# Kernel optimization log

Hardware: AMD Instinct MI355X
Metric: run time of the kernel (lower is better)

The kernel has to match this reference:

```python
import jax, jax.numpy as jnp
import numpy as np

B, L, D, M = 8, 4096, 512, 64


def setup_inputs() -> dict:
    key = jax.random.key(0)
    k1, k2, k3 = jax.random.split(key, 3)
    scale = 1.0 / (D * D)
    return {
        "q": jax.random.normal(k1, (B, L, D), dtype=jnp.float32),
        "w_real": scale * jax.random.normal(k2, (D, D, M), dtype=jnp.float32),
        "w_imag": scale * jax.random.normal(k3, (D, D, M), dtype=jnp.float32),
    }


def reference(q, w_real, w_imag):
    # q: [B, L, D]; weights: [D, D, modes]
    b, l, d = q.shape
    n_freq = l // 2 + 1
    q_ft = jnp.fft.rfft(q, axis=1)                      # [B, n_freq, D] complex64
    m = min(w_real.shape[-1], n_freq)
    W = w_real[..., :m] + 1j * w_imag[..., :m]          # [D, E, m] complex
    # Batched over modes: replaces the per-mode python loop with one einsum.
    out_m = jnp.einsum('bmd,dem->bme', q_ft[:, :m, :], W)  # [B, m, D]
    out_ft = jnp.zeros((b, n_freq, d), dtype=q_ft.dtype).at[:, :m, :].set(out_m)
    return jnp.fft.irfft(out_ft, n=l, axis=1)           # [B, L, D] float32
```

## Files before the change

### kernel.cpp

```cpp
#include <hip/hip_runtime.h>

#define B_ 8
#define L_ 4096
#define D_ 512
#define M_ 64

typedef __attribute__((ext_vector_type(8))) short bh8;
typedef __attribute__((ext_vector_type(4))) float f4;
typedef __attribute__((ext_vector_type(4))) unsigned u32x4;

__device__ inline unsigned short f2bf(float f) {
  unsigned u = __float_as_uint(f);
  return (unsigned short)((u + 0x7fffu + ((u >> 16) & 1u)) >> 16);
}
__device__ inline unsigned packbf(float lo, float hi) {
  return (unsigned)f2bf(lo) | ((unsigned)f2bf(hi) << 16);
}

__global__ void k_ftab(unsigned short* __restrict__ F) {
  int t = blockIdx.x * 256 + threadIdx.x;
  int r = t >> 12, l = t & 4095;
  int k = r & 63, part = r >> 6;
  int ph = (k * l) & (L_ - 1);
  double ang = 6.283185307179586476925286766559 * (double)ph / (double)L_;
  float v = part ? (float)(-sin(ang)) : (float)(cos(ang));
  F[t] = f2bf(v);
}

__global__ void k_gtab(unsigned short* __restrict__ G) {
  int t = blockIdx.x * 256 + threadIdx.x;
  int l = t >> 7, j = t & 127;
  int k = j & 63, part = j >> 6;
  int ph = (k * l) & (L_ - 1);
  double ang = 6.283185307179586476925286766559 * (double)ph / (double)L_;
  double ck = (k == 0 ? 1.0 : 2.0) / (double)L_;
  float v = part ? (float)(-ck * sin(ang)) : (float)(ck * cos(ang));
  G[t] = f2bf(v);
}

__global__ __launch_bounds__(512, 4) void k_dft_mfma(
    const float* __restrict__ q, const unsigned short* __restrict__ F,
    float* __restrict__ pQ) {
  int tid = threadIdx.x;
  int dt = blockIdx.x, b = blockIdx.y, kc = blockIdx.z;
  int d0 = dt * 64;
  int lbase = kc * 512;

  int w = tid >> 6, lane = tid & 63;
  int mh = w & 3, nc = w >> 2;
  int lr = lane & 15, kg = lane >> 4;

  f4 acc[2][2];
#pragma unroll
  for (int i = 0; i < 2; ++i)
#pragma unroll
    for (int j = 0; j < 2; ++j) { f4 z = {0.f, 0.f, 0.f, 0.f}; acc[i][j] = z; }

  const unsigned short* A0 = F + (size_t)(mh * 32 + lr) * 4096 + lbase + kg * 8;
  const unsigned short* A1 = A0 + (size_t)16 * 4096;
  const float* q0 = q + ((size_t)b * L_ + lbase + kg * 8) * D_ + d0 + nc * 32 + lr;

#pragma unroll 2
  for (int s = 0; s < 16; ++s) {
    const float* qs = q0 + (size_t)s * 32 * D_;
    float v0[8], v1[8];
#pragma unroll
    for (int j = 0; j < 8; ++j) {
      v0[j] = qs[(size_t)j * D_];
      v1[j] = qs[(size_t)j * D_ + 16];
    }
    union { u32x4 u; bh8 h; } bf0, bf1;
    bf0.u.x = packbf(v0[0], v0[1]); bf0.u.y = packbf(v0[2], v0[3]);
    bf0.u.z = packbf(v0[4], v0[5]); bf0.u.w = packbf(v0[6], v0[7]);
    bf1.u.x = packbf(v1[0], v1[1]); bf1.u.y = packbf(v1[2], v1[3]);
    bf1.u.z = packbf(v1[4], v1[5]); bf1.u.w = packbf(v1[6], v1[7]);
    bh8 af0 = *(const bh8*)(A0 + s * 32);
    bh8 af1 = *(const bh8*)(A1 + s * 32);
    acc[0][0] = __builtin_amdgcn_mfma_f32_16x16x32_bf16(af0, bf0.h, acc[0][0], 0, 0, 0);
    acc[0][1] = __builtin_amdgcn_mfma_f32_16x16x32_bf16(af0, bf1.h, acc[0][1], 0, 0, 0);
    acc[1][0] = __builtin_amdgcn_mfma_f32_16x16x32_bf16(af1, bf0.h, acc[1][0], 0, 0, 0);
    acc[1][1] = __builtin_amdgcn_mfma_f32_16x16x32_bf16(af1, bf1.h, acc[1][1], 0, 0, 0);
  }

#pragma unroll
  for (int mi = 0; mi < 2; ++mi) {
    int r = mh * 32 + mi * 16 + kg * 4;
#pragma unroll
    for (int ni = 0; ni < 2; ++ni) {
      int d = d0 + nc * 32 + ni * 16 + lr;
#pragma unroll
      for (int j = 0; j < 4; ++j)
        pQ[(((size_t)kc * 128 + (r + j)) * 8 + b) * 512 + d] = acc[mi][ni][j];
    }
  }
}

__global__ __launch_bounds__(256) void k_red2(const float* __restrict__ pQ,
                                              unsigned* __restrict__ Qbf) {
  int g = blockIdx.x * 256 + threadIdx.x;
  int dq = g & 127;
  int b = (g >> 7) & 7;
  int k = g >> 10;
  f4 sr = {0.f, 0.f, 0.f, 0.f}, si = {0.f, 0.f, 0.f, 0.f};
#pragma unroll
  for (int kc = 0; kc < 8; ++kc) {
    size_t base = (((size_t)kc * 128 + k) * 8 + b) * 512 + dq * 4;
    sr += *(const f4*)(pQ + base);
    si += *(const f4*)(pQ + base + (size_t)64 * 8 * 512);
  }
  u32x4 o;
  o.x = packbf(sr[0], si[0]); o.y = packbf(sr[1], si[1]);
  o.z = packbf(sr[2], si[2]); o.w = packbf(sr[3], si[3]);
  *(u32x4*)(Qbf + ((size_t)k * 8 + b) * 512 + dq * 4) = o;
}

__global__ __launch_bounds__(512, 4) void k_mix_mfma(
    const float* __restrict__ wr_, const float* __restrict__ wi_,
    const unsigned* __restrict__ Qbf, float* __restrict__ pOut) {
  __shared__ unsigned Wt[16384];
  int tid = threadIdx.x;
  int et = blockIdx.x, dc = blockIdx.y;
  int e0 = et * 16;
  int w = tid >> 6, lane = tid & 63;
  int er = lane & 15, kg = lane >> 4;
  int part = er >> 3, b = er & 7;

  f4 acc[8];
#pragma unroll
  for (int t = 0; t < 8; ++t) { f4 z = {0.f, 0.f, 0.f, 0.f}; acc[t] = z; }

  for (int r = 0; r < 4; ++r) {
    if (r) __syncthreads();
    int dbase = dc * 64 + r * 16;
#pragma unroll
    for (int i = 0; i < 8; ++i) {
      int f = tid + i * 512;
      int d_loc = f >> 8;
      int e = (f >> 4) & 15;
      int k4 = f & 15;
      size_t gidx = ((size_t)(dbase + d_loc) * 512 + (e0 + e)) * 16 + k4;
      float4 a  = ((const float4*)wr_)[gidx];
      float4 bb = ((const float4*)wi_)[gidx];
      int dp = d_loc ^ ((k4 & 3) << 2);
      int base = k4 * 1024 + e * 16 + dp;
      Wt[base]       = packbf(a.x, bb.x);
      Wt[base + 256] = packbf(a.y, bb.y);
      Wt[base + 512] = packbf(a.z, bb.z);
      Wt[base + 768] = packbf(a.w, bb.w);
    }
    __syncthreads();
    int d0 = dbase + kg * 4;
#pragma unroll
    for (int t = 0; t < 8; ++t) {
      int k = w * 8 + t;
      int sw = ((k >> 2) & 3) << 2;
      union { u32x4 u; bh8 h; } av, bv;
      av.u = *(const u32x4*)&Wt[k * 256 + er * 16 + ((kg * 4) ^ sw)];
      u32x4 qv = *(const u32x4*)(Qbf + ((size_t)k * 8 + b) * 512 + d0);
      if (part == 0) {
        bv.u.x = qv.x ^ 0x80000000u; bv.u.y = qv.y ^ 0x80000000u;
        bv.u.z = qv.z ^ 0x80000000u; bv.u.w = qv.w ^ 0x80000000u;
      } else {
        bv.u.x = (qv.x >> 16) | (qv.x << 16); bv.u.y = (qv.y >> 16) | (qv.y << 16);
        bv.u.z = (qv.z >> 16) | (qv.z << 16); bv.u.w = (qv.w >> 16) | (qv.w << 16);
      }
      acc[t] = __builtin_amdgcn_mfma_f32_16x16x32_bf16(av.h, bv.h, acc[t], 0, 0, 0);
    }
  }

#pragma unroll
  for (int t = 0; t < 8; ++t) {
    int k = w * 8 + t;
    size_t off = (size_t)dc * 524288 +
                 (((size_t)k * 2 + part) * 8 + b) * 512 + e0 + kg * 4;
    *(f4*)(pOut + off) = acc[t];
  }
}

__global__ __launch_bounds__(256) void k_psum2(const float* __restrict__ pOut,
                                               unsigned* __restrict__ Pw) {
  __shared__ float sP[128 * 33];
  int tid = threadIdx.x;
  int e0 = blockIdx.x * 32, b = blockIdx.y;
  {
    int e = tid & 31, kg4 = tid >> 5;
#pragma unroll
    for (int ii = 0; ii < 16; ++ii) {
      int col = kg4 * 16 + ii;
      int rkp = ((col & 63) << 1) | (col >> 6);
      float s = 0.f;
#pragma unroll
      for (int c = 0; c < 8; ++c)
        s += pOut[(size_t)c * 524288 + (size_t)rkp * 4096 + b * 512 + e0 + e];
      sP[col * 33 + e] = s;
    }
  }
  __syncthreads();
  {
    int e = tid >> 3, c = tid & 7;
    size_t wbase = (((size_t)b * 512 + e0 + e) * 128 + c * 16) >> 1;
#pragma unroll
    for (int ii = 0; ii < 8; ++ii) {
      int col = c * 16 + ii * 2;
      Pw[wbase + ii] = packbf(sP[col * 33 + e], sP[(col + 1) * 33 + e]);
    }
  }
}

#define LST 72
__global__ __launch_bounds__(256, 2) void k_inv_mfma(
    const short* __restrict__ G, const short* __restrict__ P,
    float* __restrict__ y) {
  __shared__ short lds[2 * 128 * LST];
  short* As = lds;
  short* Bs = lds + 128 * LST;

  int tid = threadIdx.x;
  int lt = blockIdx.x, et = blockIdx.y, b = blockIdx.z;
  int l0 = lt * 128, e0 = et * 128;

  int wv = tid >> 6, lane = tid & 63;
  int wrow = wv >> 1, wcol = wv & 1;
  int lr = lane & 15, kg = lane >> 4;

  const short* Gb = G + (size_t)l0 * 128;
  const short* Pb = P + (size_t)b * D_ * 128 + (size_t)e0 * 128;

  f4 acc[4][4];
#pragma unroll
  for (int mi = 0; mi < 4; ++mi)
#pragma unroll
    for (int ni = 0; ni < 4; ++ni) {
      f4 z = {0.f, 0.f, 0.f, 0.f};
      acc[mi][ni] = z;
    }

#pragma unroll
  for (int kh = 0; kh < 2; ++kh) {
    if (kh) __syncthreads();
#pragma unroll
    for (int i = 0; i < 4; ++i) {
      int idx = i * 256 + tid;
      int row = idx >> 3, c = idx & 7;
      *(uint4*)(As + row * LST + c * 8) =
          *(const uint4*)(Gb + (size_t)row * 128 + kh * 64 + c * 8);
      *(uint4*)(Bs + row * LST + c * 8) =
          *(const uint4*)(Pb + (size_t)row * 128 + kh * 64 + c * 8);
    }
    __syncthreads();

#pragma unroll
    for (int ks = 0; ks < 2; ++ks) {
      bh8 a[4], bf[4];
#pragma unroll
      for (int i = 0; i < 4; ++i) {
        a[i]  = *(const bh8*)(As + (wrow * 64 + i * 16 + lr) * LST + ks * 32 + kg * 8);
        bf[i] = *(const bh8*)(Bs + (wcol * 64 + i * 16 + lr) * LST + ks * 32 + kg * 8);
      }
#pragma unroll
      for (int mi = 0; mi < 4; ++mi)
#pragma unroll
        for (int ni = 0; ni < 4; ++ni)
          acc[mi][ni] = __builtin_amdgcn_mfma_f32_16x16x32_bf16(
              a[mi], bf[ni], acc[mi][ni], 0, 0, 0);
    }
  }

#pragma unroll
  for (int mi = 0; mi < 4; ++mi) {
    int lg = l0 + wrow * 64 + mi * 16 + kg * 4;
#pragma unroll
    for (int ni = 0; ni < 4; ++ni) {
      int e = e0 + wcol * 64 + ni * 16 + lr;
#pragma unroll
      for (int j = 0; j < 4; ++j)
        y[((size_t)b * L_ + (lg + j)) * D_ + e] = acc[mi][ni][j];
    }
  }
}

extern "C" void kernel_launch(void* const* d_in, const int* in_sizes, int n_in,
                              void* d_out, int out_size, void* d_ws, size_t ws_size,
                              hipStream_t stream) {
  const float* q  = (const float*)d_in[0];
  const float* wr = (const float*)d_in[1];
  const float* wi = (const float*)d_in[2];
  float* out = (float*)d_out;
  char* ws = (char*)d_ws;

  unsigned short* Fbf = (unsigned short*)ws;
  unsigned short* Gbf = (unsigned short*)(ws + (1u << 20));
  unsigned* Qbf       = (unsigned*)(ws + (2u << 20));
  unsigned* Pw        = (unsigned*)(ws + (3u << 20));

  float* pQ   = out;
  float* pOut = out;

  hipLaunchKernelGGL(k_ftab, dim3((128 * L_) / 256), dim3(256), 0, stream, Fbf);
  hipLaunchKernelGGL(k_gtab, dim3((L_ * 128) / 256), dim3(256), 0, stream, Gbf);
  hipLaunchKernelGGL(k_dft_mfma, dim3(8, 8, 8), dim3(512), 0, stream,
                     q, Fbf, pQ);
  hipLaunchKernelGGL(k_red2, dim3(65536 / 256), dim3(256), 0, stream, pQ, Qbf);
  hipLaunchKernelGGL(k_mix_mfma, dim3(D_ / 16, 8), dim3(512), 0, stream,
                     wr, wi, Qbf, pOut);
  hipLaunchKernelGGL(k_psum2, dim3(16, 8), dim3(256), 0, stream, pOut, Pw);
  hipLaunchKernelGGL(k_inv_mfma, dim3(L_ / 128, D_ / 128, B_), dim3(256), 0,
                     stream, (const short*)Gbf, (const short*)Pw, out);
}
```

Before: 107.7 us.

## Double-buffer weight loads in mix kernel and split D reduction across more blocks

The mix kernel now covers 32 input channels per block instead of 64, which doubles the grid to 16 D-chunks so more blocks stream the 64 MB of weights in parallel. Inside each block, the global loads for the second 16-channel slab are issued into registers before the MFMA work on the first slab, so load latency overlaps compute. The partial-sum kernel now reduces 16 partial outputs instead of 8, which means more partial traffic through the output buffer. Register pressure also rises from holding 16 float4 values per thread.

```diff
diff --git a/kernel.cpp b/kernel.cpp
--- a/kernel.cpp
+++ b/kernel.cpp
@@ -125,48 +125,65 @@
   int er = lane & 15, kg = lane >> 4;
   int part = er >> 3, b = er & 7;
 
+  int e = (tid >> 4) & 15, k4 = tid & 15, dl0 = tid >> 8;
+  const float4* wr4p = (const float4*)wr_;
+  const float4* wi4p = (const float4*)wi_;
+  int dbase = dc * 32;
+
   f4 acc[8];
 #pragma unroll
   for (int t = 0; t < 8; ++t) { f4 z = {0.f, 0.f, 0.f, 0.f}; acc[t] = z; }
 
-  for (int r = 0; r < 4; ++r) {
-    if (r) __syncthreads();
-    int dbase = dc * 64 + r * 16;
-#pragma unroll
-    for (int i = 0; i < 8; ++i) {
-      int f = tid + i * 512;
-      int d_loc = f >> 8;
-      int e = (f >> 4) & 15;
-      int k4 = f & 15;
-      size_t gidx = ((size_t)(dbase + d_loc) * 512 + (e0 + e)) * 16 + k4;
-      float4 a  = ((const float4*)wr_)[gidx];
-      float4 bb = ((const float4*)wi_)[gidx];
-      int dp = d_loc ^ ((k4 & 3) << 2);
-      int base = k4 * 1024 + e * 16 + dp;
-      Wt[base]       = packbf(a.x, bb.x);
-      Wt[base + 256] = packbf(a.y, bb.y);
-      Wt[base + 512] = packbf(a.z, bb.z);
-      Wt[base + 768] = packbf(a.w, bb.w);
-    }
-    __syncthreads();
-    int d0 = dbase + kg * 4;
-#pragma unroll
-    for (int t = 0; t < 8; ++t) {
-      int k = w * 8 + t;
-      int sw = ((k >> 2) & 3) << 2;
-      union { u32x4 u; bh8 h; } av, bv;
-      av.u = *(const u32x4*)&Wt[k * 256 + er * 16 + ((kg * 4) ^ sw)];
-      u32x4 qv = *(const u32x4*)(Qbf + ((size_t)k * 8 + b) * 512 + d0);
-      if (part == 0) {
-        bv.u.x = qv.x ^ 0x80000000u; bv.u.y = qv.y ^ 0x80000000u;
-        bv.u.z = qv.z ^ 0x80000000u; bv.u.w = qv.w ^ 0x80000000u;
-      } else {
-        bv.u.x = (qv.x >> 16) | (qv.x << 16); bv.u.y = (qv.y >> 16) | (qv.y << 16);
-        bv.u.z = (qv.z >> 16) | (qv.z << 16); bv.u.w = (qv.w >> 16) | (qv.w << 16);
-      }
-      acc[t] = __builtin_amdgcn_mfma_f32_16x16x32_bf16(av.h, bv.h, acc[t], 0, 0, 0);
-    }
-  }
+  float4 wrv[8], wiv[8];
+
+#define GOFF(dd) ((((size_t)(dd)*512) + e0 + e) * 16 + k4)
+#define LOADW(dstart)                                   \
+  _Pragma("unroll") for (int i = 0; i < 8; ++i) {       \
+    int dd = (dstart) + dl0 + 2 * i;                    \
+    wrv[i] = wr4p[GOFF(dd)];                            \
+    wiv[i] = wi4p[GOFF(dd)];                            \
+  }
+#define PACKW()                                         \
+  _Pragma("unroll") for (int i = 0; i < 8; ++i) {       \
+    int d_loc = dl0 + 2 * i;                            \
+    int dp = d_loc ^ ((k4 & 3) << 2);                   \
+    int base = k4 * 1024 + e * 16 + dp;                 \
+    Wt[base]       = packbf(wrv[i].x, wiv[i].x);        \
+    Wt[base + 256] = packbf(wrv[i].y, wiv[i].y);        \
+    Wt[base + 512] = packbf(wrv[i].z, wiv[i].z);        \
+    Wt[base + 768] = packbf(wrv[i].w, wiv[i].w);        \
+  }
+#define COMPUTEW(dq)                                                        \
+  _Pragma("unroll") for (int t = 0; t < 8; ++t) {                           \
+    int k = w * 8 + t;                                                      \
+    int sw = ((k >> 2) & 3) << 2;                                           \
+    union { u32x4 u; bh8 h; } av, bv;                                       \
+    av.u = *(const u32x4*)&Wt[k * 256 + er * 16 + ((kg * 4) ^ sw)];         \
+    u32x4 qv = *(const u32x4*)(Qbf + ((size_t)k * 8 + b) * 512 + (dq) + kg * 4); \
+    if (part == 0) {                                                        \
+      bv.u.x = qv.x ^ 0x80000000u; bv.u.y = qv.y ^ 0x80000000u;             \
+      bv.u.z = qv.z ^ 0x80000000u; bv.u.w = qv.w ^ 0x80000000u;             \
+    } else {                                                                \
+      bv.u.x = (qv.x >> 16) | (qv.x << 16); bv.u.y = (qv.y >> 16) | (qv.y << 16); \
+      bv.u.z = (qv.z >> 16) | (qv.z << 16); bv.u.w = (qv.w >> 16) | (qv.w << 16); \
+    }                                                                       \
+    acc[t] = __builtin_amdgcn_mfma_f32_16x16x32_bf16(av.h, bv.h, acc[t], 0, 0, 0); \
+  }
+
+  LOADW(dbase);
+  PACKW();
+  __syncthreads();
+  LOADW(dbase + 16);
+  COMPUTEW(dbase);
+  __syncthreads();
+  PACKW();
+  __syncthreads();
+  COMPUTEW(dbase + 16);
+
+#undef GOFF
+#undef LOADW
+#undef PACKW
+#undef COMPUTEW
 
 #pragma unroll
   for (int t = 0; t < 8; ++t) {
@@ -190,7 +207,7 @@
       int rkp = ((col & 63) << 1) | (col >> 6);
       float s = 0.f;
 #pragma unroll
-      for (int c = 0; c < 8; ++c)
+      for (int c = 0; c < 16; ++c)
         s += pOut[(size_t)c * 524288 + (size_t)rkp * 4096 + b * 512 + e0 + e];
       sP[col * 33 + e] = s;
     }
@@ -301,7 +318,7 @@
   hipLaunchKernelGGL(k_dft_mfma, dim3(8, 8, 8), dim3(512), 0, stream,
                      q, Fbf, pQ);
   hipLaunchKernelGGL(k_red2, dim3(65536 / 256), dim3(256), 0, stream, pQ, Qbf);
-  hipLaunchKernelGGL(k_mix_mfma, dim3(D_ / 16, 8), dim3(512), 0, stream,
+  hipLaunchKernelGGL(k_mix_mfma, dim3(D_ / 16, 16), dim3(512), 0, stream,
                      wr, wi, Qbf, pOut);
   hipLaunchKernelGGL(k_psum2, dim3(16, 8), dim3(256), 0, stream, pOut, Pw);
   hipLaunchKernelGGL(k_inv_mfma, dim3(L_ / 128, D_ / 128, B_), dim3(256), 0,
```

Measured after the change: 127.3 us. 1.18x slower.

## Software-pipeline mode-mixing kernel with double-buffered LDS and split mode dimension

Applied to the files above, without the earlier changes.

Rewrites the weight-mixing MFMA kernel so each block handles half of the 64 modes, which doubles the grid and halves the per-block accumulators. Weight loads use inline-asm global loads that are double-buffered in LDS with manual vmcnt/lgkmcnt waits and barriers, so loading the next d-slice overlaps with the MFMA work on the current one. The load pattern also changes so each lane reads contiguous mode runs. The gain is more parallelism and hidden weight-streaming latency. The cost is fragile hand-counted waitcnts and inline asm that the compiler cannot schedule around.

```diff
diff --git a/kernel.cpp b/kernel.cpp
--- a/kernel.cpp
+++ b/kernel.cpp
@@ -117,62 +117,144 @@
 __global__ __launch_bounds__(512, 4) void k_mix_mfma(
     const float* __restrict__ wr_, const float* __restrict__ wi_,
     const unsigned* __restrict__ Qbf, float* __restrict__ pOut) {
-  __shared__ unsigned Wt[16384];
+  __shared__ unsigned Wt[2][8192];
+
   int tid = threadIdx.x;
-  int et = blockIdx.x, dc = blockIdx.y;
-  int e0 = et * 16;
+  int et = blockIdx.x, kh = blockIdx.y, dc = blockIdx.z;
+  int e0 = et * 16, D0 = dc * 64;
   int w = tid >> 6, lane = tid & 63;
   int er = lane & 15, kg = lane >> 4;
   int part = er >> 3, b = er & 7;
 
-  f4 acc[8];
-#pragma unroll
-  for (int t = 0; t < 8; ++t) { f4 z = {0.f, 0.f, 0.f, 0.f}; acc[t] = z; }
-
-  for (int r = 0; r < 4; ++r) {
-    if (r) __syncthreads();
-    int dbase = dc * 64 + r * 16;
-#pragma unroll
-    for (int i = 0; i < 8; ++i) {
-      int f = tid + i * 512;
-      int d_loc = f >> 8;
-      int e = (f >> 4) & 15;
-      int k4 = f & 15;
-      size_t gidx = ((size_t)(dbase + d_loc) * 512 + (e0 + e)) * 16 + k4;
-      float4 a  = ((const float4*)wr_)[gidx];
-      float4 bb = ((const float4*)wi_)[gidx];
-      int dp = d_loc ^ ((k4 & 3) << 2);
-      int base = k4 * 1024 + e * 16 + dp;
-      Wt[base]       = packbf(a.x, bb.x);
-      Wt[base + 256] = packbf(a.y, bb.y);
-      Wt[base + 512] = packbf(a.z, bb.z);
-      Wt[base + 768] = packbf(a.w, bb.w);
-    }
-    __syncthreads();
-    int d0 = dbase + kg * 4;
-#pragma unroll
-    for (int t = 0; t < 8; ++t) {
-      int k = w * 8 + t;
-      int sw = ((k >> 2) & 3) << 2;
-      union { u32x4 u; bh8 h; } av, bv;
-      av.u = *(const u32x4*)&Wt[k * 256 + er * 16 + ((kg * 4) ^ sw)];
-      u32x4 qv = *(const u32x4*)(Qbf + ((size_t)k * 8 + b) * 512 + d0);
-      if (part == 0) {
-        bv.u.x = qv.x ^ 0x80000000u; bv.u.y = qv.y ^ 0x80000000u;
-        bv.u.z = qv.z ^ 0x80000000u; bv.u.w = qv.w ^ 0x80000000u;
-      } else {
-        bv.u.x = (qv.x >> 16) | (qv.x << 16); bv.u.y = (qv.y >> 16) | (qv.y << 16);
-        bv.u.z = (qv.z >> 16) | (qv.z << 16); bv.u.w = (qv.w >> 16) | (qv.w << 16);
-      }
-      acc[t] = __builtin_amdgcn_mfma_f32_16x16x32_bf16(av.h, bv.h, acc[t], 0, 0, 0);
-    }
-  }
-
-#pragma unroll
-  for (int t = 0; t < 8; ++t) {
-    int k = w * 8 + t;
+  int e8 = lane >> 3, k4g = lane & 7;
+  int koff = kh * 32 + k4g * 4;
+  int swl = (k4g & 3) << 2;
+  int dloc0 = w * 2;
+
+  const unsigned* qlane =
+      Qbf + ((size_t)(kh * 32 + w * 4) * 8 + b) * 512 + D0 + kg * 4;
+
+  f4 acc[4];
+#pragma unroll
+  for (int t = 0; t < 4; ++t) { f4 z = {0.f, 0.f, 0.f, 0.f}; acc[t] = z; }
+
+  f4 LR0, LR1, LR2, LR3, LI0, LI1, LI2, LI3;
+  u32x4 QA0, QA1, QA2, QA3, QB0, QB1, QB2, QB3;
+
+#define GLD(dst, p) \
+  asm volatile("global_load_dwordx4 %0, %1, off" : "=v"(dst) : "v"(p))
+#define SB() __builtin_amdgcn_sched_barrier(0)
+#define VMW(n) do { asm volatile("s_waitcnt vmcnt(" #n ")" ::: "memory"); SB(); } while (0)
+#define LKM0() do { asm volatile("s_waitcnt lgkmcnt(0)" ::: "memory"); SB(); } while (0)
+#define BAR() do { __builtin_amdgcn_s_barrier(); SB(); } while (0)
+
+#define LOADL(r) do {                                                        \
+    size_t d_ = (size_t)(D0 + 16 * (r) + dloc0);                             \
+    const float* p00 = wr_ + (d_ * 512 + e0 + e8) * 64 + koff;               \
+    const float* p01 = wr_ + (d_ * 512 + e0 + 8 + e8) * 64 + koff;           \
+    const float* p10 = wr_ + ((d_ + 1) * 512 + e0 + e8) * 64 + koff;         \
+    const float* p11 = wr_ + ((d_ + 1) * 512 + e0 + 8 + e8) * 64 + koff;     \
+    const float* q00 = wi_ + (d_ * 512 + e0 + e8) * 64 + koff;               \
+    const float* q01 = wi_ + (d_ * 512 + e0 + 8 + e8) * 64 + koff;           \
+    const float* q10 = wi_ + ((d_ + 1) * 512 + e0 + e8) * 64 + koff;         \
+    const float* q11 = wi_ + ((d_ + 1) * 512 + e0 + 8 + e8) * 64 + koff;     \
+    GLD(LR0, p00); GLD(LR1, p01); GLD(LR2, p10); GLD(LR3, p11);              \
+    GLD(LI0, q00); GLD(LI1, q01); GLD(LI2, q10); GLD(LI3, q11);              \
+  } while (0)
+
+#define LOADQ(q0_, q1_, q2_, q3_, r) do {                                    \
+    GLD(q0_, (const float*)(qlane + (r) * 16));                              \
+    GLD(q1_, (const float*)(qlane + 4096 + (r) * 16));                       \
+    GLD(q2_, (const float*)(qlane + 8192 + (r) * 16));                       \
+    GLD(q3_, (const float*)(qlane + 12288 + (r) * 16));                      \
+  } while (0)
+
+#define PACK1(wb, vr, vi, dl, el) do {                                       \
+    int dp_ = (dl) ^ swl;                                                    \
+    unsigned* o_ = &Wt[wb][(k4g * 4) * 256 + (el) * 16 + dp_];               \
+    o_[0]   = packbf(vr[0], vi[0]);                                          \
+    o_[256] = packbf(vr[1], vi[1]);                                          \
+    o_[512] = packbf(vr[2], vi[2]);                                          \
+    o_[768] = packbf(vr[3], vi[3]);                                          \
+  } while (0)
+
+#define PACKL(wb) do {                                                      \
+    PACK1(wb, LR0, LI0, dloc0, e8);                                         \
+    PACK1(wb, LR1, LI1, dloc0, 8 + e8);                                     \
+    PACK1(wb, LR2, LI2, dloc0 + 1, e8);                                     \
+    PACK1(wb, LR3, LI3, dloc0 + 1, 8 + e8);                                 \
+  } while (0)
+
+#define COMPW(wb, q0_, q1_, q2_, q3_) do {                                  \
+    u32x4 qarr0 = q0_, qarr1 = q1_, qarr2 = q2_, qarr3 = q3_;               \
+    _Pragma("unroll") for (int t = 0; t < 4; ++t) {                         \
+      int kl_ = w * 4 + t;                                                  \
+      int sw_ = ((kl_ >> 2) & 3) << 2;                                      \
+      union { u32x4 u; bh8 h; } av, bv;                                     \
+      av.u = *(const u32x4*)&Wt[wb][kl_ * 256 + er * 16 + ((kg * 4) ^ sw_)]; \
+      u32x4 q = (t == 0) ? qarr0 : (t == 1) ? qarr1 : (t == 2) ? qarr2 : qarr3; \
+      if (part == 0) {                                                      \
+        bv.u.x = q.x ^ 0x80000000u; bv.u.y = q.y ^ 0x80000000u;             \
+        bv.u.z = q.z ^ 0x80000000u; bv.u.w = q.w ^ 0x80000000u;             \
+      } else {                                                              \
+        bv.u.x = (q.x >> 16) | (q.x << 16); bv.u.y = (q.y >> 16) | (q.y << 16); \
+        bv.u.z = (q.z >> 16) | (q.z << 16); bv.u.w = (q.w >> 16) | (q.w << 16); \
+      }                                                                     \
+      acc[t] = __builtin_amdgcn_mfma_f32_16x16x32_bf16(av.h, bv.h, acc[t], 0, 0, 0); \
+    }                                                                       \
+  } while (0)
+
+  LOADL(0);
+  VMW(0);
+  PACKL(0);
+  LOADL(1);
+  LOADQ(QA0, QA1, QA2, QA3, 0);
+
+  VMW(4);
+  PACKL(1);
+  LKM0(); BAR();
+  LOADL(2);
+  LOADQ(QB0, QB1, QB2, QB3, 1);
+  VMW(12);
+  COMPW(0, QA0, QA1, QA2, QA3);
+  LKM0(); BAR();
+
+  VMW(4);
+  PACKL(0);
+  LKM0(); BAR();
+  LOADL(3);
+  LOADQ(QA0, QA1, QA2, QA3, 2);
+  VMW(12);
+  COMPW(1, QB0, QB1, QB2, QB3);
+  LKM0(); BAR();
+
+  VMW(4);
+  PACKL(1);
+  LKM0(); BAR();
+  LOADQ(QB0, QB1, QB2, QB3, 3);
+  VMW(4);
+  COMPW(0, QA0, QA1, QA2, QA3);
+  LKM0(); BAR();
+
+  VMW(0);
+  COMPW(1, QB0, QB1, QB2, QB3);
+
+#undef GLD
+#undef SB
+#undef VMW
+#undef LKM0
+#undef BAR
+#undef LOADL
+#undef LOADQ
+#undef PACK1
+#undef PACKL
+#undef COMPW
+
+#pragma unroll
+  for (int t = 0; t < 4; ++t) {
+    int kglob = kh * 32 + w * 4 + t;
     size_t off = (size_t)dc * 524288 +
-                 (((size_t)k * 2 + part) * 8 + b) * 512 + e0 + kg * 4;
+                 (((size_t)kglob * 2 + part) * 8 + b) * 512 + e0 + kg * 4;
     *(f4*)(pOut + off) = acc[t];
   }
 }
@@ -301,7 +383,7 @@
   hipLaunchKernelGGL(k_dft_mfma, dim3(8, 8, 8), dim3(512), 0, stream,
                      q, Fbf, pQ);
   hipLaunchKernelGGL(k_red2, dim3(65536 / 256), dim3(256), 0, stream, pQ, Qbf);
-  hipLaunchKernelGGL(k_mix_mfma, dim3(D_ / 16, 8), dim3(512), 0, stream,
+  hipLaunchKernelGGL(k_mix_mfma, dim3(32, 2, 8), dim3(512), 0, stream,
                      wr, wi, Qbf, pOut);
   hipLaunchKernelGGL(k_psum2, dim3(16, 8), dim3(256), 0, stream, pOut, Pw);
   hipLaunchKernelGGL(k_inv_mfma, dim3(L_ / 128, D_ / 128, B_), dim3(256), 0,
```

After: 101.3 us. 6.0% less time.

## Split mode-mixing kernel across modes and finer D chunks for more blocks

Applied to the files above, without the earlier changes.

The mixing kernel grid grows from 256 blocks of 512 threads to 2048 blocks of 256 threads. Each block now handles 16 output features, 32 input features and 16 modes, with a smaller shared tile. The point is to keep more blocks resident per CU so the bandwidth-bound 128MB weight stream has better latency hiding. In exchange there are 16 partial-sum slices instead of 8, which doubles the partial-sum traffic written by the mixer and read back in k_psum2. Each weight read also becomes a shorter contiguous segment.

```diff
diff --git a/kernel.cpp b/kernel.cpp
--- a/kernel.cpp
+++ b/kernel.cpp
@@ -114,49 +114,52 @@
   *(u32x4*)(Qbf + ((size_t)k * 8 + b) * 512 + dq * 4) = o;
 }
 
-__global__ __launch_bounds__(512, 4) void k_mix_mfma(
+__global__ __launch_bounds__(256, 5) void k_mix_mfma(
     const float* __restrict__ wr_, const float* __restrict__ wi_,
     const unsigned* __restrict__ Qbf, float* __restrict__ pOut) {
-  __shared__ unsigned Wt[16384];
+  __shared__ unsigned Wt[4096];
+
   int tid = threadIdx.x;
-  int et = blockIdx.x, dc = blockIdx.y;
-  int e0 = et * 16;
+  int et = blockIdx.x, dc = blockIdx.y, kq = blockIdx.z;
+  int e0 = et * 16, D0 = dc * 32, k0 = kq * 16;
   int w = tid >> 6, lane = tid & 63;
   int er = lane & 15, kg = lane >> 4;
   int part = er >> 3, b = er & 7;
 
-  f4 acc[8];
-#pragma unroll
-  for (int t = 0; t < 8; ++t) { f4 z = {0.f, 0.f, 0.f, 0.f}; acc[t] = z; }
-
-  for (int r = 0; r < 4; ++r) {
+  int se = tid & 15;
+  int sk4 = (tid >> 4) & 3;
+  int sdg = tid >> 6;
+
+  f4 acc[4];
+#pragma unroll
+  for (int t = 0; t < 4; ++t) { f4 z = {0.f, 0.f, 0.f, 0.f}; acc[t] = z; }
+
+#pragma unroll 1
+  for (int r = 0; r < 2; ++r) {
     if (r) __syncthreads();
-    int dbase = dc * 64 + r * 16;
-#pragma unroll
-    for (int i = 0; i < 8; ++i) {
-      int f = tid + i * 512;
-      int d_loc = f >> 8;
-      int e = (f >> 4) & 15;
-      int k4 = f & 15;
-      size_t gidx = ((size_t)(dbase + d_loc) * 512 + (e0 + e)) * 16 + k4;
-      float4 a  = ((const float4*)wr_)[gidx];
-      float4 bb = ((const float4*)wi_)[gidx];
-      int dp = d_loc ^ ((k4 & 3) << 2);
-      int base = k4 * 1024 + e * 16 + dp;
-      Wt[base]       = packbf(a.x, bb.x);
-      Wt[base + 256] = packbf(a.y, bb.y);
-      Wt[base + 512] = packbf(a.z, bb.z);
-      Wt[base + 768] = packbf(a.w, bb.w);
+#pragma unroll
+    for (int i = 0; i < 4; ++i) {
+      int dl = sdg * 4 + i;
+      size_t dd = (size_t)(D0 + r * 16 + dl);
+      size_t gb = (dd * 512 + e0 + se) * 64 + k0 + sk4 * 4;
+      float4 vr = *(const float4*)(wr_ + gb);
+      float4 vi = *(const float4*)(wi_ + gb);
+      int dp = dl ^ (sk4 << 2);
+      unsigned* o = &Wt[(sk4 * 4) * 256 + se * 16 + dp];
+      o[0]   = packbf(vr.x, vi.x);
+      o[256] = packbf(vr.y, vi.y);
+      o[512] = packbf(vr.z, vi.z);
+      o[768] = packbf(vr.w, vi.w);
     }
     __syncthreads();
-    int d0 = dbase + kg * 4;
-#pragma unroll
-    for (int t = 0; t < 8; ++t) {
-      int k = w * 8 + t;
-      int sw = ((k >> 2) & 3) << 2;
+#pragma unroll
+    for (int t = 0; t < 4; ++t) {
+      int kl = w * 4 + t;
+      int sw = (kl >> 2) << 2;
       union { u32x4 u; bh8 h; } av, bv;
-      av.u = *(const u32x4*)&Wt[k * 256 + er * 16 + ((kg * 4) ^ sw)];
-      u32x4 qv = *(const u32x4*)(Qbf + ((size_t)k * 8 + b) * 512 + d0);
+      av.u = *(const u32x4*)&Wt[kl * 256 + er * 16 + ((kg * 4) ^ sw)];
+      u32x4 qv = *(const u32x4*)(Qbf +
+          ((size_t)(k0 + kl) * 8 + b) * 512 + D0 + r * 16 + kg * 4);
       if (part == 0) {
         bv.u.x = qv.x ^ 0x80000000u; bv.u.y = qv.y ^ 0x80000000u;
         bv.u.z = qv.z ^ 0x80000000u; bv.u.w = qv.w ^ 0x80000000u;
@@ -169,10 +172,10 @@
   }
 
 #pragma unroll
-  for (int t = 0; t < 8; ++t) {
-    int k = w * 8 + t;
+  for (int t = 0; t < 4; ++t) {
+    int kglob = k0 + w * 4 + t;
     size_t off = (size_t)dc * 524288 +
-                 (((size_t)k * 2 + part) * 8 + b) * 512 + e0 + kg * 4;
+                 (((size_t)kglob * 2 + part) * 8 + b) * 512 + e0 + kg * 4;
     *(f4*)(pOut + off) = acc[t];
   }
 }
@@ -190,7 +193,7 @@
       int rkp = ((col & 63) << 1) | (col >> 6);
       float s = 0.f;
 #pragma unroll
-      for (int c = 0; c < 8; ++c)
+      for (int c = 0; c < 16; ++c)
         s += pOut[(size_t)c * 524288 + (size_t)rkp * 4096 + b * 512 + e0 + e];
       sP[col * 33 + e] = s;
     }
@@ -301,7 +304,7 @@
   hipLaunchKernelGGL(k_dft_mfma, dim3(8, 8, 8), dim3(512), 0, stream,
                      q, Fbf, pQ);
   hipLaunchKernelGGL(k_red2, dim3(65536 / 256), dim3(256), 0, stream, pQ, Qbf);
-  hipLaunchKernelGGL(k_mix_mfma, dim3(D_ / 16, 8), dim3(512), 0, stream,
+  hipLaunchKernelGGL(k_mix_mfma, dim3(32, 16, 4), dim3(256), 0, stream,
                      wr, wi, Qbf, pOut);
   hipLaunchKernelGGL(k_psum2, dim3(16, 8), dim3(256), 0, stream, pOut, Pw);
   hipLaunchKernelGGL(k_inv_mfma, dim3(L_ / 128, D_ / 128, B_), dim3(256), 0,
```

After: 113.7 us. 1.06x slower.
